# Kernel tuning notes

Hardware: AMD Instinct MI355X
Metric: run time of the kernel (lower is better)

## Reference

```python
import jax, jax.numpy as jnp
import numpy as np

N_LAYERS = 10
PS_SQ = 1            # patch_size^2
D = 3 * PS_SQ        # feature dim = 3
AFFINE_EPS = 1e-4
LOG2PI = float(np.log(2.0 * np.pi))


def setup_inputs() -> dict:
    key = jax.random.key(0)
    ks = jax.random.split(key, 6)
    N = 2_097_152
    x = jax.random.normal(ks[0], (N, D), dtype=jnp.float32)
    affine_info = jax.random.normal(ks[1], (N, N_LAYERS * 2 * D), dtype=jnp.float32)
    # NaiveLinear params per layer (invertible linear y = x @ W + b).
    # Init near identity so the flow stays well-conditioned/invertible.
    Ws = jnp.eye(D, dtype=jnp.float32)[None] + 0.05 * jax.random.normal(ks[2], (N_LAYERS, D, D), dtype=jnp.float32)
    bs = 0.05 * jax.random.normal(ks[3], (N_LAYERS, D), dtype=jnp.float32)
    last_W = jnp.eye(D, dtype=jnp.float32) + 0.05 * jax.random.normal(ks[4], (D, D), dtype=jnp.float32)
    last_b = 0.05 * jax.random.normal(ks[5], (D,), dtype=jnp.float32)
    return {"x": x, "affine_info": affine_info, "Ws": Ws, "bs": bs,
            "last_W": last_W, "last_b": last_b}


def reference(x, affine_info, Ws, bs, last_W, last_b):
    z = x
    total_log_det = jnp.zeros((x.shape[0],), dtype=x.dtype)
    for i in range(N_LAYERS):
        W, b = Ws[i], bs[i]
        # NaiveLinear: y = z @ W + b, logdet = log|det W| (same for every sample)
        z = z @ W + b
        total_log_det = total_log_det + jnp.linalg.slogdet(W)[1].astype(x.dtype)
        # affine coupling driven by conditioning slice [N, 2D]
        sl = affine_info[:, i * 2 * D:(i + 1) * 2 * D]
        scale_raw, shift = sl[:, :D], sl[:, D:]
        scale = jax.nn.sigmoid(scale_raw + 2.0) + AFFINE_EPS
        z = z * scale + shift
        total_log_det = total_log_det + jnp.sum(jnp.log(scale), axis=-1)
    z = z @ last_W + last_b
    total_log_det = total_log_det + jnp.linalg.slogdet(last_W)[1].astype(x.dtype)
    total_log_det = total_log_det + jnp.sum(-0.5 * (z * z + LOG2PI), axis=-1)
    return z, total_log_det
```

## Files before the change

### kernel.cpp

```cpp
#include <hip/hip_runtime.h>
#include <math.h>

#define NUM_LAYERS 10

#define AF_PAD 61

__device__ __forceinline__ float det3(const float* __restrict__ W) {
    return W[0] * (W[4] * W[8] - W[5] * W[7])
         - W[1] * (W[3] * W[8] - W[5] * W[6])
         + W[2] * (W[3] * W[7] - W[4] * W[6]);
}

__global__ __launch_bounds__(64) void flow_kernel(
    const float* __restrict__ x,
    const float* __restrict__ affine,
    const float* __restrict__ Ws,
    const float* __restrict__ bs,
    const float* __restrict__ lastW,
    const float* __restrict__ lastb,
    float* __restrict__ out_z,
    float* __restrict__ out_ld,
    int N)
{
    __shared__ float lds_af[64 * AF_PAD];

    const int tid = threadIdx.x;
    const int row0 = blockIdx.x * 64;

    const float4* ap = reinterpret_cast<const float4*>(affine) + (size_t)blockIdx.x * 960;
    float4 v[15];
#pragma unroll
    for (int k = 0; k < 15; ++k) v[k] = ap[k * 64 + tid];
#pragma unroll
    for (int k = 0; k < 15; ++k) {
        const int idx = k * 64 + tid;
        const int r   = idx / 15;
        const int e4  = idx - r * 15;
        float* p = &lds_af[r * AF_PAD + e4 * 4];
        p[0] = v[k].x; p[1] = v[k].y; p[2] = v[k].z; p[3] = v[k].w;
    }
    __syncthreads();

    const int row = row0 + tid;
    if (row >= N) return;

    float const_ld = 0.0f;
#pragma unroll
    for (int i = 0; i < NUM_LAYERS; ++i) {
        const_ld += logf(fabsf(det3(Ws + i * 9)));
    }
    const_ld += logf(fabsf(det3(lastW)));

    const float LOG2PI = 1.8378770664093453f;
    const float AFFINE_EPS = 1e-4f;

    float z0 = x[(size_t)row * 3 + 0];
    float z1 = x[(size_t)row * 3 + 1];
    float z2 = x[(size_t)row * 3 + 2];

    const float* af = &lds_af[tid * AF_PAD];
    float ld = 0.0f;

#pragma unroll
    for (int i = 0; i < NUM_LAYERS; ++i) {
        const float* W = Ws + i * 9;
        const float* b = bs + i * 3;
        float n0 = fmaf(z0, W[0], fmaf(z1, W[3], fmaf(z2, W[6], b[0])));
        float n1 = fmaf(z0, W[1], fmaf(z1, W[4], fmaf(z2, W[7], b[1])));
        float n2 = fmaf(z0, W[2], fmaf(z1, W[5], fmaf(z2, W[8], b[2])));

        const float s0 = af[i * 6 + 0];
        const float s1 = af[i * 6 + 1];
        const float s2 = af[i * 6 + 2];
        const float t0 = af[i * 6 + 3];
        const float t1 = af[i * 6 + 4];
        const float t2 = af[i * 6 + 5];

        const float sc0 = 1.0f / (1.0f + expf(-(s0 + 2.0f))) + AFFINE_EPS;
        const float sc1 = 1.0f / (1.0f + expf(-(s1 + 2.0f))) + AFFINE_EPS;
        const float sc2 = 1.0f / (1.0f + expf(-(s2 + 2.0f))) + AFFINE_EPS;

        z0 = fmaf(n0, sc0, t0);
        z1 = fmaf(n1, sc1, t1);
        z2 = fmaf(n2, sc2, t2);

        ld += logf(sc0) + logf(sc1) + logf(sc2);
    }

    {
        const float* W = lastW;
        float n0 = fmaf(z0, W[0], fmaf(z1, W[3], fmaf(z2, W[6], lastb[0])));
        float n1 = fmaf(z0, W[1], fmaf(z1, W[4], fmaf(z2, W[7], lastb[1])));
        float n2 = fmaf(z0, W[2], fmaf(z1, W[5], fmaf(z2, W[8], lastb[2])));
        z0 = n0; z1 = n1; z2 = n2;
    }

    ld += const_ld;
    ld += -0.5f * (z0 * z0 + LOG2PI)
        + -0.5f * (z1 * z1 + LOG2PI)
        + -0.5f * (z2 * z2 + LOG2PI);

    out_z[(size_t)row * 3 + 0] = z0;
    out_z[(size_t)row * 3 + 1] = z1;
    out_z[(size_t)row * 3 + 2] = z2;
    out_ld[row] = ld;
}

extern "C" void kernel_launch(void* const* d_in, const int* in_sizes, int n_in,
                              void* d_out, int out_size, void* d_ws, size_t ws_size,
                              hipStream_t stream) {
    const float* x      = (const float*)d_in[0];
    const float* affine = (const float*)d_in[1];
    const float* Ws     = (const float*)d_in[2];
    const float* bs     = (const float*)d_in[3];
    const float* lastW  = (const float*)d_in[4];
    const float* lastb  = (const float*)d_in[5];

    const int N = in_sizes[0] / 3;

    float* out_z  = (float*)d_out;
    float* out_ld = (float*)d_out + (size_t)N * 3;

    const int block = 64;
    const int grid = (N + block - 1) / block;
    flow_kernel<<<grid, block, 0, stream>>>(x, affine, Ws, bs, lastW, lastb,
                                            out_z, out_ld, N);
}
```

Measured before the change: 684.7 us.

## Precompute constant logdet, stage x via LDS, use fast intrinsics and batched logs

Adds a one-thread prep kernel that computes the constant log-determinant sum (plus the Gaussian constant) into workspace, so each thread reads one float instead of computing eleven 3x3 determinants and logs. The x rows are loaded as coalesced float4s into LDS rather than strided scalar loads. The sigmoid uses fast __expf and a hardware reciprocal, and the per-layer logs are merged by multiplying scales two layers at a time before one __logf. This lowers ALU and transcendental cost but adds an extra kernel launch and slightly reduces numerical accuracy. The x LDS staging assumes N is a multiple of 64.

After: 678.5 us. No clear change (-0.9%).

```diff
diff --git a/kernel.cpp b/kernel.cpp
--- a/kernel.cpp
+++ b/kernel.cpp
@@ -11,6 +11,24 @@
          + W[2] * (W[3] * W[7] - W[4] * W[6]);
 }
 
+__device__ __forceinline__ float const_logdet(const float* __restrict__ Ws,
+                                              const float* __restrict__ lastW) {
+    float cld = 0.0f;
+#pragma unroll
+    for (int i = 0; i < NUM_LAYERS; ++i) {
+        cld += __logf(fabsf(det3(Ws + i * 9)));
+    }
+    cld += __logf(fabsf(det3(lastW)));
+    cld += -1.5f * 1.8378770664093453f;
+    return cld;
+}
+
+__global__ void prep_kernel(const float* __restrict__ Ws,
+                            const float* __restrict__ lastW,
+                            float* __restrict__ out) {
+    *out = const_logdet(Ws, lastW);
+}
+
 __global__ __launch_bounds__(64) void flow_kernel(
     const float* __restrict__ x,
     const float* __restrict__ affine,
@@ -18,11 +36,13 @@
     const float* __restrict__ bs,
     const float* __restrict__ lastW,
     const float* __restrict__ lastb,
+    const float* __restrict__ cld_ptr,
     float* __restrict__ out_z,
     float* __restrict__ out_ld,
     int N)
 {
     __shared__ float lds_af[64 * AF_PAD];
+    __shared__ float lds_x[64 * 3];
 
     const int tid = threadIdx.x;
     const int row0 = blockIdx.x * 64;
@@ -31,6 +51,10 @@
     float4 v[15];
 #pragma unroll
     for (int k = 0; k < 15; ++k) v[k] = ap[k * 64 + tid];
+
+    float4 xv;
+    if (tid < 48) xv = reinterpret_cast<const float4*>(x)[(size_t)blockIdx.x * 48 + tid];
+
 #pragma unroll
     for (int k = 0; k < 15; ++k) {
         const int idx = k * 64 + tid;
@@ -39,52 +63,49 @@
         float* p = &lds_af[r * AF_PAD + e4 * 4];
         p[0] = v[k].x; p[1] = v[k].y; p[2] = v[k].z; p[3] = v[k].w;
     }
+    if (tid < 48) {
+        float* p = &lds_x[tid * 4];
+        p[0] = xv.x; p[1] = xv.y; p[2] = xv.z; p[3] = xv.w;
+    }
     __syncthreads();
 
     const int row = row0 + tid;
     if (row >= N) return;
 
-    float const_ld = 0.0f;
-#pragma unroll
-    for (int i = 0; i < NUM_LAYERS; ++i) {
-        const_ld += logf(fabsf(det3(Ws + i * 9)));
-    }
-    const_ld += logf(fabsf(det3(lastW)));
+    const float cld = cld_ptr ? *cld_ptr : const_logdet(Ws, lastW);
 
-    const float LOG2PI = 1.8378770664093453f;
     const float AFFINE_EPS = 1e-4f;
 
-    float z0 = x[(size_t)row * 3 + 0];
-    float z1 = x[(size_t)row * 3 + 1];
-    float z2 = x[(size_t)row * 3 + 2];
+    float z0 = lds_x[tid * 3 + 0];
+    float z1 = lds_x[tid * 3 + 1];
+    float z2 = lds_x[tid * 3 + 2];
 
     const float* af = &lds_af[tid * AF_PAD];
     float ld = 0.0f;
 
 #pragma unroll
-    for (int i = 0; i < NUM_LAYERS; ++i) {
-        const float* W = Ws + i * 9;
-        const float* b = bs + i * 3;
-        float n0 = fmaf(z0, W[0], fmaf(z1, W[3], fmaf(z2, W[6], b[0])));
-        float n1 = fmaf(z0, W[1], fmaf(z1, W[4], fmaf(z2, W[7], b[1])));
-        float n2 = fmaf(z0, W[2], fmaf(z1, W[5], fmaf(z2, W[8], b[2])));
+    for (int ii = 0; ii < NUM_LAYERS; ii += 2) {
+        float prod = 1.0f;
+#pragma unroll
+        for (int j = 0; j < 2; ++j) {
+            const int i = ii + j;
+            const float* W = Ws + i * 9;
+            const float* b = bs + i * 3;
+            float n0 = fmaf(z0, W[0], fmaf(z1, W[3], fmaf(z2, W[6], b[0])));
+            float n1 = fmaf(z0, W[1], fmaf(z1, W[4], fmaf(z2, W[7], b[1])));
+            float n2 = fmaf(z0, W[2], fmaf(z1, W[5], fmaf(z2, W[8], b[2])));
 
-        const float s0 = af[i * 6 + 0];
-        const float s1 = af[i * 6 + 1];
-        const float s2 = af[i * 6 + 2];
-        const float t0 = af[i * 6 + 3];
-        const float t1 = af[i * 6 + 4];
-        const float t2 = af[i * 6 + 5];
+            const float sc0 = __builtin_amdgcn_rcpf(1.0f + __expf(-(af[i * 6 + 0] + 2.0f))) + AFFINE_EPS;
+            const float sc1 = __builtin_amdgcn_rcpf(1.0f + __expf(-(af[i * 6 + 1] + 2.0f))) + AFFINE_EPS;
+            const float sc2 = __builtin_amdgcn_rcpf(1.0f + __expf(-(af[i * 6 + 2] + 2.0f))) + AFFINE_EPS;
 
-        const float sc0 = 1.0f / (1.0f + expf(-(s0 + 2.0f))) + AFFINE_EPS;
-        const float sc1 = 1.0f / (1.0f + expf(-(s1 + 2.0f))) + AFFINE_EPS;
-        const float sc2 = 1.0f / (1.0f + expf(-(s2 + 2.0f))) + AFFINE_EPS;
+            z0 = fmaf(n0, sc0, af[i * 6 + 3]);
+            z1 = fmaf(n1, sc1, af[i * 6 + 4]);
+            z2 = fmaf(n2, sc2, af[i * 6 + 5]);
 
-        z0 = fmaf(n0, sc0, t0);
-        z1 = fmaf(n1, sc1, t1);
-        z2 = fmaf(n2, sc2, t2);
-
-        ld += logf(sc0) + logf(sc1) + logf(sc2);
+            prod *= sc0 * sc1 * sc2;
+        }
+        ld += __logf(prod);
     }
 
     {
@@ -95,10 +116,7 @@
         z0 = n0; z1 = n1; z2 = n2;
     }
 
-    ld += const_ld;
-    ld += -0.5f * (z0 * z0 + LOG2PI)
-        + -0.5f * (z1 * z1 + LOG2PI)
-        + -0.5f * (z2 * z2 + LOG2PI);
+    ld += cld - 0.5f * (z0 * z0 + z1 * z1 + z2 * z2);
 
     out_z[(size_t)row * 3 + 0] = z0;
     out_z[(size_t)row * 3 + 1] = z1;
@@ -121,8 +139,13 @@
     float* out_z  = (float*)d_out;
     float* out_ld = (float*)d_out + (size_t)N * 3;
 
+    float* cld_ws = (d_ws != nullptr && ws_size >= sizeof(float)) ? (float*)d_ws : nullptr;
+    if (cld_ws) {
+        prep_kernel<<<1, 1, 0, stream>>>(Ws, lastW, cld_ws);
+    }
+
     const int block = 64;
     const int grid = (N + block - 1) / block;
     flow_kernel<<<grid, block, 0, stream>>>(x, affine, Ws, bs, lastW, lastb,
-                                            out_z, out_ld, N);
+                                            cld_ws, out_z, out_ld, N);
 }
```
